# Kernel optimization log

Measured on AMD Instinct MI355X. Metric: run time of the kernel, lower is better.

## Reference

```python
import jax, jax.numpy as jnp
import numpy as np

H = 16  # num heads
DH = 64  # head dim


def setup_inputs() -> dict:
    key = jax.random.key(0)
    ks = jax.random.split(key, 9)
    d = 1024
    s = 0.02
    return {
        "hidden_states": jax.random.normal(ks[0], (16, 1024, d), jnp.float32),
        "Wq": jax.random.normal(ks[1], (d, d), jnp.float32) * s,
        "bq": jax.random.normal(ks[2], (d,), jnp.float32) * s,
        "Wk": jax.random.normal(ks[3], (d, d), jnp.float32) * s,
        "bk": jax.random.normal(ks[4], (d,), jnp.float32) * s,
        "Wv": jax.random.normal(ks[5], (d, d), jnp.float32) * s,
        "bv": jax.random.normal(ks[6], (d,), jnp.float32) * s,
        "Wo": jax.random.normal(ks[7], (d, d), jnp.float32) * s,
        "bo": jax.random.normal(ks[8], (d,), jnp.float32) * s,
    }


def _heads(x):
    b, s, _ = x.shape
    return x.reshape(b, s, H, DH).transpose(0, 2, 1, 3)  # [B,H,S,Dh]


def reference(hidden_states, Wq, bq, Wk, bk, Wv, bv, Wo, bo):
    # torch nn.Linear: y = x @ W.T + b; weights here are [out, in]
    q = _heads(hidden_states @ Wq.T + bq)
    k = _heads(hidden_states @ Wk.T + bk)
    v = _heads(hidden_states @ Wv.T + bv)
    scores = jnp.einsum("bhqd,bhkd->bhqk", q, k) / jnp.sqrt(jnp.float32(DH))
    probs = jax.nn.softmax(scores, axis=-1)
    ctx = jnp.einsum("bhqk,bhkd->bhqd", probs, v)
    b, _, s, _ = ctx.shape
    ctx = ctx.transpose(0, 2, 1, 3).reshape(b, s, H * DH)
    out = ctx @ Wo.T + bo
    # module returns (attention_output, weights=None); return array only
    return out
```

## Files before the change

### kernel.cpp

```cpp
#include <hip/hip_runtime.h>
#include <hip/hip_bf16.h>
#include <stdint.h>


typedef short bf16x8 __attribute__((ext_vector_type(8)));
typedef float f32x4 __attribute__((ext_vector_type(4)));
typedef float f32x16 __attribute__((ext_vector_type(16)));
typedef unsigned short ushort_t;
typedef ushort_t us8 __attribute__((ext_vector_type(8)));

__device__ __forceinline__ ushort_t f2b(float f) {
    unsigned x;
    __builtin_memcpy(&x, &f, 4);
    unsigned r = (x + 0x7fffu + ((x >> 16) & 1u)) >> 16;
    return (ushort_t)r;
}

__device__ __forceinline__ void glds16(const void* g, void* l) {
    __builtin_amdgcn_global_load_lds(
        (const __attribute__((address_space(1))) void*)g,
        (__attribute__((address_space(3))) void*)l, 16, 0, 0);
}

#define MFMA16(a, b, c) __builtin_amdgcn_mfma_f32_16x16x32_bf16((a), (b), (c), 0, 0, 0)
#define MFMA32(a, b, c) __builtin_amdgcn_mfma_f32_32x32x16_bf16((a), (b), (c), 0, 0, 0)

__global__ __launch_bounds__(256, 8) void cvt4_kernel(
    const float* __restrict__ s0, const float* __restrict__ s1,
    const float* __restrict__ s2, const float* __restrict__ s3,
    ushort_t* __restrict__ d0, ushort_t* __restrict__ d1,
    ushort_t* __restrict__ d2, ushort_t* __restrict__ d3, int n8)
{
    const float* in = (blockIdx.y == 0) ? s0 : (blockIdx.y == 1) ? s1
                       : (blockIdx.y == 2) ? s2 : s3;
    ushort_t* out = (blockIdx.y == 0) ? d0 : (blockIdx.y == 1) ? d1
                       : (blockIdx.y == 2) ? d2 : d3;
    int i = blockIdx.x * 256 + threadIdx.x;
    if (i >= n8) return;
    const float4* p = (const float4*)in + (size_t)i * 2;
    float4 a = p[0], b = p[1];
    us8 v;
    v[0] = f2b(a.x); v[1] = f2b(a.y); v[2] = f2b(a.z); v[3] = f2b(a.w);
    v[4] = f2b(b.x); v[5] = f2b(b.y); v[6] = f2b(b.z); v[7] = f2b(b.w);
    *((us8*)out + i) = v;
}

__global__ __launch_bounds__(256, 8) void cvt1_kernel(
    const float* __restrict__ in, ushort_t* __restrict__ out, int n8)
{
    int i = blockIdx.x * 256 + threadIdx.x;
    if (i >= n8) return;
    const float4* p = (const float4*)in + (size_t)i * 2;
    float4 a = p[0], b = p[1];
    us8 v;
    v[0] = f2b(a.x); v[1] = f2b(a.y); v[2] = f2b(a.z); v[3] = f2b(a.w);
    v[4] = f2b(b.x); v[5] = f2b(b.y); v[6] = f2b(b.z); v[7] = f2b(b.w);
    *((us8*)out + i) = v;
}

template <bool OUTF>
__global__ __launch_bounds__(512) void gemm256_kernel(
    const ushort_t* __restrict__ A,
    const ushort_t* __restrict__ W0, const ushort_t* __restrict__ W1, const ushort_t* __restrict__ W2,
    const float* __restrict__ b0, const float* __restrict__ b1, const float* __restrict__ b2,
    void* __restrict__ C0, void* __restrict__ C1, void* __restrict__ C2,
    float s0, float s1, float s2, int N, int K)
{
    const ushort_t* W = (blockIdx.z == 0) ? W0 : ((blockIdx.z == 1) ? W1 : W2);
    const float* bias = (blockIdx.z == 0) ? b0 : ((blockIdx.z == 1) ? b1 : b2);
    void* C = (blockIdx.z == 0) ? C0 : ((blockIdx.z == 1) ? C1 : C2);
    const float scale = (blockIdx.z == 0) ? s0 : ((blockIdx.z == 1) ? s1 : s2);

    __shared__ ushort_t lds[2][4][256 * 32];

    const int tid = threadIdx.x;
    const int lane = tid & 63;
    const int wave = tid >> 6;
    const int wr = wave >> 2;
    const int wc = wave & 3;
    const int r32 = lane & 31;
    const int g = lane >> 5;

    const int gx = gridDim.x;
    const int flat = blockIdx.y * gx + blockIdx.x;
    const int cpx = (gx * gridDim.y) >> 3;
    const int swz = (flat & 7) * cpx + (flat >> 3);
    const int bm = (swz % gx) * 256;
    const int bn = (swz / gx) * 256;

    const ushort_t* Ag = A + (size_t)bm * K;
    const ushort_t* Bg = W + (size_t)bn * K;

    const int q0 = tid, q1 = 512 + tid;
    const int sr0 = q0 >> 2, sc0 = (((q0 & 3) - (sr0 >> 1)) & 3) * 8;
    const int sr1 = q1 >> 2, sc1 = (((q1 & 3) - (sr1 >> 1)) & 3) * 8;

#define STG(gbase, kcol, dst) do { \
    glds16((gbase) + (size_t)sr0 * K + (kcol) + sc0, (dst) + q0 * 8); \
    glds16((gbase) + (size_t)sr1 * K + (kcol) + sc1, (dst) + q1 * 8); } while (0)

#define BARRIER() do { \
    __builtin_amdgcn_sched_barrier(0); \
    asm volatile("s_barrier" ::: "memory"); \
    __builtin_amdgcn_sched_barrier(0); } while (0)

#define VMCNT(n) asm volatile("s_waitcnt vmcnt(" #n ")" ::: "memory")

#define ROT(r, c) (((((c) + ((r) >> 1)) & 3)) * 8)

    f32x16 acc[4][2] = {};
    bf16x8 af[2][2], bfr[2][2];

#define LDA(buf, kh, mh) do { _Pragma("unroll") \
    for (int i = 0; i < 2; ++i) { _Pragma("unroll") \
        for (int t = 0; t < 2; ++t) { \
            int row = wr * 128 + ((mh) * 2 + i) * 32 + r32; \
            af[i][t] = *(const bf16x8*)(&lds[buf][kh][0] + row * 32 + ROT(row, 2 * t + g)); \
        } } } while (0)
#define LDB(buf, kh) do { _Pragma("unroll") \
    for (int ni = 0; ni < 2; ++ni) { _Pragma("unroll") \
        for (int t = 0; t < 2; ++t) { \
            int row = wc * 64 + ni * 32 + r32; \
            bfr[ni][t] = *(const bf16x8*)(&lds[buf][2 + (kh)][0] + row * 32 + ROT(row, 2 * t + g)); \
        } } } while (0)
#define MM(mh) do { __builtin_amdgcn_s_setprio(1); _Pragma("unroll") \
    for (int i = 0; i < 2; ++i) { _Pragma("unroll") \
        for (int ni = 0; ni < 2; ++ni) { \
            acc[(mh) * 2 + i][ni] = MFMA32(af[i][0], bfr[ni][0], acc[(mh) * 2 + i][ni]); \
            acc[(mh) * 2 + i][ni] = MFMA32(af[i][1], bfr[ni][1], acc[(mh) * 2 + i][ni]); \
        } } \
    __builtin_amdgcn_s_setprio(0); } while (0)

    STG(Ag, 0,  &lds[0][0][0]);
    STG(Bg, 0,  &lds[0][2][0]);
    STG(Ag, 32, &lds[0][1][0]);
    STG(Bg, 32, &lds[0][3][0]);
    STG(Bg, 64, &lds[1][2][0]);
    STG(Ag, 64, &lds[1][0][0]);
    VMCNT(4);
    BARRIER();

#pragma unroll 1
    for (int i = 0; i < 7; ++i) {
        const int t = 2 * i;
        const int kc1 = (t + 1) * 64, kc2 = (t + 2) * 64, kc3 = (t + 3) * 64;
        LDB(0, 0); LDA(0, 0, 0);
        STG(Bg, kc1 + 32, &lds[1][3][0]);
        BARRIER(); MM(0);
        LDA(0, 0, 1);
        STG(Ag, kc1 + 32, &lds[1][1][0]);
        VMCNT(8);
        BARRIER(); MM(1);
        LDB(0, 1); LDA(0, 1, 0);
        STG(Bg, kc2, &lds[0][2][0]);
        BARRIER(); MM(0);
        LDA(0, 1, 1);
        STG(Ag, kc2, &lds[0][0][0]);
        VMCNT(8);
        BARRIER(); MM(1);
        LDB(1, 0); LDA(1, 0, 0);
        STG(Bg, kc2 + 32, &lds[0][3][0]);
        BARRIER(); MM(0);
        LDA(1, 0, 1);
        STG(Ag, kc2 + 32, &lds[0][1][0]);
        VMCNT(8);
        BARRIER(); MM(1);
        LDB(1, 1); LDA(1, 1, 0);
        STG(Bg, kc3, &lds[1][2][0]);
        BARRIER(); MM(0);
        LDA(1, 1, 1);
        STG(Ag, kc3, &lds[1][0][0]);
        VMCNT(8);
        BARRIER(); MM(1);
    }

    {
        const int kc15 = 15 * 64;
        LDB(0, 0); LDA(0, 0, 0);
        STG(Bg, kc15 + 32, &lds[1][3][0]);
        BARRIER(); MM(0);
        LDA(0, 0, 1);
        STG(Ag, kc15 + 32, &lds[1][1][0]);
        VMCNT(8);
        BARRIER(); MM(1);
        LDB(0, 1); LDA(0, 1, 0);
        BARRIER(); MM(0);
        LDA(0, 1, 1);
        VMCNT(0);
        BARRIER(); MM(1);
        LDB(1, 0); LDA(1, 0, 0); MM(0);
        LDA(1, 0, 1); MM(1);
        LDB(1, 1); LDA(1, 1, 0); MM(0);
        LDA(1, 1, 1); MM(1);
    }

#pragma unroll
    for (int ni = 0; ni < 2; ++ni) {
        const int col = bn + wc * 64 + ni * 32 + r32;
        const float bv = bias[col];
#pragma unroll
        for (int mi = 0; mi < 4; ++mi) {
            const int rbase = bm + wr * 128 + mi * 32 + 4 * g;
#pragma unroll
            for (int reg = 0; reg < 16; ++reg) {
                const int row = rbase + (reg & 3) + 8 * (reg >> 2);
                float v = (acc[mi][ni][reg] + bv) * scale;
                if (OUTF)
                    ((float*)C)[(size_t)row * N + col] = v;
                else
                    ((ushort_t*)C)[(size_t)row * N + col] = f2b(v);
            }
        }
    }
#undef STG
#undef BARRIER
#undef VMCNT
#undef ROT
#undef LDA
#undef LDB
#undef MM
}

__global__ __launch_bounds__(256, 4) void transpose_v_kernel(
    const ushort_t* __restrict__ V, ushort_t* __restrict__ Vt)
{
    __shared__ ushort_t t[64 * 65];
    const int bh = blockIdx.x;
    const int st = blockIdx.y;
    const int b = bh >> 4, h = bh & 15;
    const int tid = threadIdx.x;

#pragma unroll
    for (int i = 0; i < 16; ++i) {
        int e = i * 256 + tid;
        int s = e >> 6, d = e & 63;
        t[s * 65 + d] = V[(size_t)(b * 1024 + st * 64 + s) * 1024 + h * 64 + d];
    }
    __syncthreads();
#pragma unroll
    for (int i = 0; i < 16; ++i) {
        int e = i * 256 + tid;
        int d = e >> 6, s = e & 63;
        Vt[(size_t)(bh * 64 + d) * 1024 + st * 64 + s] = t[s * 65 + d];
    }
}

__global__ __launch_bounds__(256, 2) void attn_kernel(
    const ushort_t* __restrict__ Q, const ushort_t* __restrict__ K,
    const ushort_t* __restrict__ Vt, ushort_t* __restrict__ ctx)
{
    __shared__ ushort_t Ks[2][64 * 64];
    __shared__ ushort_t Ps[4][32 * 72];

    const int bh = blockIdx.x;
    const int qt = blockIdx.y;
    const int b = bh >> 4, h = bh & 15;
    const int tid = threadIdx.x;
    const int lane = tid & 63;
    const int wave = tid >> 6;
    const int q = lane >> 4;
    const int ml = lane & 15;

    const int cid0 = tid;
    const int cid1 = 256 + tid;
    const int r0 = cid0 >> 3, sc0 = (cid0 & 7) ^ (r0 & 7);
    const int r1 = cid1 >> 3, sc1 = (cid1 & 7) ^ (r1 & 7);
    const ushort_t* Kbase = K + (size_t)(b * 1024) * 1024 + h * 64;
    const ushort_t* Vbase = Vt + (size_t)(bh * 64) * 1024;

    bf16x8 qf[2][2];
#pragma unroll
    for (int mg = 0; mg < 2; ++mg) {
        int row = b * 1024 + qt * 128 + wave * 32 + mg * 16 + ml;
        const ushort_t* qp = Q + (size_t)row * 1024 + h * 64;
        qf[mg][0] = *(const bf16x8*)(qp + q * 8);
        qf[mg][1] = *(const bf16x8*)(qp + 32 + q * 8);
    }

    bf16x8 ones;
#pragma unroll
    for (int i = 0; i < 8; ++i) ones[i] = (short)0x3F80;

    f32x4 o[2][4] = {};
    f32x4 ls[2] = {};
    ushort_t* Pw = Ps[wave];

    glds16(Kbase + (size_t)r0 * 1024 + sc0 * 8, Ks[0] + cid0 * 8);
    glds16(Kbase + (size_t)r1 * 1024 + sc1 * 8, Ks[0] + cid1 * 8);

    for (int kt = 0; kt < 16; ++kt) {
        const int cur = kt & 1, nxt = cur ^ 1;
        __syncthreads();
        if (kt + 1 < 16) {
            const ushort_t* Kn = Kbase + (size_t)(kt + 1) * 64 * 1024;
            glds16(Kn + (size_t)r0 * 1024 + sc0 * 8, Ks[nxt] + cid0 * 8);
            glds16(Kn + (size_t)r1 * 1024 + sc1 * 8, Ks[nxt] + cid1 * 8);
        }
        const ushort_t* Kc = Ks[cur];
        const ushort_t* Vk = Vbase + kt * 64;

#pragma unroll
        for (int n = 0; n < 4; ++n) {
            int row = n * 16 + ml;
            int c0 = q ^ (row & 7);
            int c1 = (4 + q) ^ (row & 7);
            bf16x8 k0 = *(const bf16x8*)(Kc + row * 64 + c0 * 8);
            bf16x8 k1 = *(const bf16x8*)(Kc + row * 64 + c1 * 8);
#pragma unroll
            for (int mg = 0; mg < 2; ++mg) {
                f32x4 z = {};
                z = MFMA16(k0, qf[mg][0], z);
                z = MFMA16(k1, qf[mg][1], z);
                float p0 = __builtin_amdgcn_exp2f(z[0]);
                float p1 = __builtin_amdgcn_exp2f(z[1]);
                float p2 = __builtin_amdgcn_exp2f(z[2]);
                float p3 = __builtin_amdgcn_exp2f(z[3]);
                __hip_bfloat162 h01 = __float22bfloat162_rn(make_float2(p0, p1));
                __hip_bfloat162 h23 = __float22bfloat162_rn(make_float2(p2, p3));
                uint2 dd;
                __builtin_memcpy(&dd.x, &h01, 4);
                __builtin_memcpy(&dd.y, &h23, 4);
                *(uint2*)(Pw + (mg * 16 + ml) * 72 + n * 16 + q * 4) = dd;
            }
        }

        bf16x8 pf[2][2];
#pragma unroll
        for (int mg = 0; mg < 2; ++mg) {
            pf[mg][0] = *(const bf16x8*)(Pw + (mg * 16 + ml) * 72 + q * 8);
            pf[mg][1] = *(const bf16x8*)(Pw + (mg * 16 + ml) * 72 + 32 + q * 8);
            ls[mg] = MFMA16(pf[mg][0], ones, ls[mg]);
            ls[mg] = MFMA16(pf[mg][1], ones, ls[mg]);
        }
#pragma unroll
        for (int n = 0; n < 4; ++n) {
            int row = n * 16 + ml;
            bf16x8 v0 = *(const bf16x8*)(Vk + (size_t)row * 1024 + q * 8);
            bf16x8 v1 = *(const bf16x8*)(Vk + (size_t)row * 1024 + 32 + q * 8);
#pragma unroll
            for (int mg = 0; mg < 2; ++mg) {
                o[mg][n] = MFMA16(pf[mg][0], v0, o[mg][n]);
                o[mg][n] = MFMA16(pf[mg][1], v1, o[mg][n]);
            }
        }
    }

    const int orow_base = b * 1024 + qt * 128 + wave * 32;
#pragma unroll
    for (int mg = 0; mg < 2; ++mg) {
#pragma unroll
        for (int r = 0; r < 4; ++r) {
            float lv = 1.0f / ls[mg][r];
            int orow = orow_base + mg * 16 + q * 4 + r;
#pragma unroll
            for (int n = 0; n < 4; ++n) {
                ctx[(size_t)orow * 1024 + h * 64 + n * 16 + ml] =
                    f2b(o[mg][n][r] * lv);
            }
        }
    }
}

extern "C" void kernel_launch(void* const* d_in, const int* in_sizes, int n_in,
                              void* d_out, int out_size, void* d_ws, size_t ws_size,
                              hipStream_t stream)
{
    const float* X  = (const float*)d_in[0];
    const float* Wq = (const float*)d_in[1];
    const float* bq = (const float*)d_in[2];
    const float* Wk = (const float*)d_in[3];
    const float* bk = (const float*)d_in[4];
    const float* Wv = (const float*)d_in[5];
    const float* bv = (const float*)d_in[6];
    const float* Wo = (const float*)d_in[7];
    const float* bo = (const float*)d_in[8];

    const int D = 1024;
    const int M = in_sizes[0] / D;
    const int Bb = M / 1024;
    const size_t MD = (size_t)M * D;
    const size_t DD = (size_t)D * D;

    ushort_t* ws  = (ushort_t*)d_ws;
    ushort_t* Xbf = ws;
    ushort_t* Qb  = ws + MD;
    ushort_t* Kb  = ws + 2 * MD;
    ushort_t* Vb  = ws + 3 * MD;
    ushort_t* Wqb = ws + 4 * MD;
    ushort_t* Wkb = Wqb + DD;
    ushort_t* Wvb = Wkb + DD;
    ushort_t* Wob = Wvb + DD;
    ushort_t* Vtb = Xbf;
    ushort_t* ctx = Vb;

    dim3 blk(256);
    dim3 blk512(512);

    cvt1_kernel<<<(int)(MD / 8 / 256), blk, 0, stream>>>(X, Xbf, (int)(MD / 8));
    cvt4_kernel<<<dim3((int)(DD / 8 / 256), 4), blk, 0, stream>>>(
        Wq, Wk, Wv, Wo, Wqb, Wkb, Wvb, Wob, (int)(DD / 8));

    const float qscale = 1.4426950408889634f * 0.125f;
    dim3 gqkv(M / 256, D / 256, 3);
    gemm256_kernel<false><<<gqkv, blk512, 0, stream>>>(Xbf, Wqb, Wkb, Wvb,
                                                       bq, bk, bv,
                                                       Qb, Kb, Vb,
                                                       qscale, 1.0f, 1.0f, D, D);

    transpose_v_kernel<<<dim3(Bb * 16, 16), blk, 0, stream>>>(Vb, Vtb);

    attn_kernel<<<dim3(Bb * 16, 8), blk, 0, stream>>>(Qb, Kb, Vtb, ctx);

    dim3 go(M / 256, D / 256, 1);
    gemm256_kernel<true><<<go, blk512, 0, stream>>>(ctx, Wob, Wob, Wob,
                                                    bo, bo, bo,
                                                    d_out, d_out, d_out,
                                                    1.0f, 1.0f, 1.0f, D, D);
}
```

Baseline: 456.7 us.

## Stage V tiles in LDS with async double buffering and merge conversion kernels

```diff
diff --git a/kernel.cpp b/kernel.cpp
--- a/kernel.cpp
+++ b/kernel.cpp
@@ -25,31 +25,27 @@
 #define MFMA16(a, b, c) __builtin_amdgcn_mfma_f32_16x16x32_bf16((a), (b), (c), 0, 0, 0)
 #define MFMA32(a, b, c) __builtin_amdgcn_mfma_f32_32x32x16_bf16((a), (b), (c), 0, 0, 0)
 
-__global__ __launch_bounds__(256, 8) void cvt4_kernel(
-    const float* __restrict__ s0, const float* __restrict__ s1,
-    const float* __restrict__ s2, const float* __restrict__ s3,
+__global__ __launch_bounds__(256, 8) void cvt_all_kernel(
+    const float* __restrict__ X,
+    const float* __restrict__ w0, const float* __restrict__ w1,
+    const float* __restrict__ w2, const float* __restrict__ w3,
+    ushort_t* __restrict__ dx,
     ushort_t* __restrict__ d0, ushort_t* __restrict__ d1,
-    ushort_t* __restrict__ d2, ushort_t* __restrict__ d3, int n8)
+    ushort_t* __restrict__ d2, ushort_t* __restrict__ d3, int nbx)
 {
-    const float* in = (blockIdx.y == 0) ? s0 : (blockIdx.y == 1) ? s1
-                       : (blockIdx.y == 2) ? s2 : s3;
-    ushort_t* out = (blockIdx.y == 0) ? d0 : (blockIdx.y == 1) ? d1
-                       : (blockIdx.y == 2) ? d2 : d3;
-    int i = blockIdx.x * 256 + threadIdx.x;
-    if (i >= n8) return;
-    const float4* p = (const float4*)in + (size_t)i * 2;
-    float4 a = p[0], b = p[1];
-    us8 v;
-    v[0] = f2b(a.x); v[1] = f2b(a.y); v[2] = f2b(a.z); v[3] = f2b(a.w);
-    v[4] = f2b(b.x); v[5] = f2b(b.y); v[6] = f2b(b.z); v[7] = f2b(b.w);
-    *((us8*)out + i) = v;
-}
-
-__global__ __launch_bounds__(256, 8) void cvt1_kernel(
-    const float* __restrict__ in, ushort_t* __restrict__ out, int n8)
-{
-    int i = blockIdx.x * 256 + threadIdx.x;
-    if (i >= n8) return;
+    const int bid = blockIdx.x;
+    const float* in;
+    ushort_t* out;
+    int i;
+    if (bid < nbx) {
+        in = X; out = dx; i = bid * 256 + threadIdx.x;
+    } else {
+        const int w = (bid - nbx) >> 9;
+        const int sub = (bid - nbx) & 511;
+        in  = (w == 0) ? w0 : (w == 1) ? w1 : (w == 2) ? w2 : w3;
+        out = (w == 0) ? d0 : (w == 1) ? d1 : (w == 2) ? d2 : d3;
+        i = sub * 256 + threadIdx.x;
+    }
     const float4* p = (const float4*)in + (size_t)i * 2;
     float4 a = p[0], b = p[1];
     us8 v;
@@ -250,6 +246,7 @@
     const ushort_t* __restrict__ Vt, ushort_t* __restrict__ ctx)
 {
     __shared__ ushort_t Ks[2][64 * 64];
+    __shared__ ushort_t Vs[2][64 * 64];
     __shared__ ushort_t Ps[4][32 * 72];
 
     const int bh = blockIdx.x;
@@ -286,18 +283,23 @@
     ushort_t* Pw = Ps[wave];
 
     glds16(Kbase + (size_t)r0 * 1024 + sc0 * 8, Ks[0] + cid0 * 8);
+    glds16(Vbase + (size_t)r0 * 1024 + sc0 * 8, Vs[0] + cid0 * 8);
     glds16(Kbase + (size_t)r1 * 1024 + sc1 * 8, Ks[0] + cid1 * 8);
+    glds16(Vbase + (size_t)r1 * 1024 + sc1 * 8, Vs[0] + cid1 * 8);
 
     for (int kt = 0; kt < 16; ++kt) {
         const int cur = kt & 1, nxt = cur ^ 1;
         __syncthreads();
         if (kt + 1 < 16) {
             const ushort_t* Kn = Kbase + (size_t)(kt + 1) * 64 * 1024;
+            const ushort_t* Vn = Vbase + (kt + 1) * 64;
             glds16(Kn + (size_t)r0 * 1024 + sc0 * 8, Ks[nxt] + cid0 * 8);
+            glds16(Vn + (size_t)r0 * 1024 + sc0 * 8, Vs[nxt] + cid0 * 8);
             glds16(Kn + (size_t)r1 * 1024 + sc1 * 8, Ks[nxt] + cid1 * 8);
+            glds16(Vn + (size_t)r1 * 1024 + sc1 * 8, Vs[nxt] + cid1 * 8);
         }
         const ushort_t* Kc = Ks[cur];
-        const ushort_t* Vk = Vbase + kt * 64;
+        const ushort_t* Vc = Vs[cur];
 
 #pragma unroll
         for (int n = 0; n < 4; ++n) {
@@ -335,8 +337,10 @@
 #pragma unroll
         for (int n = 0; n < 4; ++n) {
             int row = n * 16 + ml;
-            bf16x8 v0 = *(const bf16x8*)(Vk + (size_t)row * 1024 + q * 8);
-            bf16x8 v1 = *(const bf16x8*)(Vk + (size_t)row * 1024 + 32 + q * 8);
+            int c0 = q ^ (row & 7);
+            int c1 = (4 + q) ^ (row & 7);
+            bf16x8 v0 = *(const bf16x8*)(Vc + row * 64 + c0 * 8);
+            bf16x8 v1 = *(const bf16x8*)(Vc + row * 64 + c1 * 8);
 #pragma unroll
             for (int mg = 0; mg < 2; ++mg) {
                 o[mg][n] = MFMA16(pf[mg][0], v0, o[mg][n]);
@@ -396,9 +400,10 @@
     dim3 blk(256);
     dim3 blk512(512);
 
-    cvt1_kernel<<<(int)(MD / 8 / 256), blk, 0, stream>>>(X, Xbf, (int)(MD / 8));
-    cvt4_kernel<<<dim3((int)(DD / 8 / 256), 4), blk, 0, stream>>>(
-        Wq, Wk, Wv, Wo, Wqb, Wkb, Wvb, Wob, (int)(DD / 8));
+    const int nbx = (int)(MD / 8 / 256);
+    const int nbw = (int)(DD / 8 / 256);
+    cvt_all_kernel<<<nbx + 4 * nbw, blk, 0, stream>>>(
+        X, Wq, Wk, Wv, Wo, Xbf, Wqb, Wkb, Wvb, Wob, nbx);
 
     const float qscale = 1.4426950408889634f * 0.125f;
     dim3 gqkv(M / 256, D / 256, 3);
```

Measured after the change: 411.3 us. 9.9% less time.
